# Kernel tuning notes

Hardware: AMD Instinct MI355X
Metric: run time of the kernel (lower is better)

## Reference

```python
import jax, jax.numpy as jnp
import numpy as np
from jax import lax

B, S, C = 64, 256, 12          # sentences, words/sentence, chars/word
Ec, Hc = 50, 64                # char embed / char LSTM hidden (per direction)
Ew = 300                       # word embed dim
Hw = 256 + Hc                  # word LSTM hidden per direction = word_hidden_dim + char_hidden_dim
Din = Ew + 2 * Hc              # word LSTM input dim
NT = 20                        # len(tag_vocab.stoi) - 2
Vw, Vc = 50000, 100


def setup_inputs() -> dict:
    key = jax.random.key(0)
    ks = jax.random.split(key, 32)
    p = lambda i, shape: jax.random.normal(ks[i], shape, jnp.float32) * 0.05
    inp = {
        'batch_sentences': jax.random.randint(ks[0], (B, S), 0, Vw),
        'lengths': jnp.full((B,), S, dtype=jnp.int32),  # sorted (all full) -> packed == time-major
        'char_ids': jax.random.randint(ks[1], (B, S, C), 0, Vc),
        'word_emb': p(2, (Vw, Ew)),
        'char_emb': p(3, (Vc, Ec)),
        'char_h0': p(4, (2, Hc)),  # fixed random init state (init_char_hidden), [fwd/bwd, Hc]
        'char_c0': p(5, (2, Hc)),
        'Wih_cf': p(6, (4 * Hc, Ec)), 'Whh_cf': p(7, (4 * Hc, Hc)), 'bih_cf': p(8, (4 * Hc,)), 'bhh_cf': p(9, (4 * Hc,)),
        'Wih_cb': p(10, (4 * Hc, Ec)), 'Whh_cb': p(11, (4 * Hc, Hc)), 'bih_cb': p(12, (4 * Hc,)), 'bhh_cb': p(13, (4 * Hc,)),
        'Wih_wf': p(14, (4 * Hw, Din)), 'Whh_wf': p(15, (4 * Hw, Hw)), 'bih_wf': p(16, (4 * Hw,)), 'bhh_wf': p(17, (4 * Hw,)),
        'Wih_wb': p(18, (4 * Hw, Din)), 'Whh_wb': p(19, (4 * Hw, Hw)), 'bih_wb': p(20, (4 * Hw,)), 'bhh_wb': p(21, (4 * Hw,)),
        'W_tag': p(22, (NT, 2 * Hw)), 'b_tag': p(23, (NT,)),
    }
    return inp


def _lstm(x, h0, c0, Wih, Whh, bih, bhh):
    """x: [T, N, In] time-major. Returns (all h [T,N,H], final h [N,H]). torch gate order i,f,g,o."""
    pre = jnp.einsum('tni,gi->tng', x, Wih) + bih  # input projection for all steps

    def step(carry, pt):
        h, c = carry
        g = pt + h @ Whh.T + bhh
        i, f, gg, o = jnp.split(g, 4, axis=-1)
        c = jax.nn.sigmoid(f) * c + jax.nn.sigmoid(i) * jnp.tanh(gg)
        h = jax.nn.sigmoid(o) * jnp.tanh(c)
        return (h, c), h

    (hT, _), hs = lax.scan(step, (h0, c0), pre)
    return hs, hT


def reference(batch_sentences, lengths, char_ids, word_emb, char_emb, char_h0, char_c0,
              Wih_cf, Whh_cf, bih_cf, bhh_cf, Wih_cb, Whh_cb, bih_cb, bhh_cb,
              Wih_wf, Whh_wf, bih_wf, bhh_wf, Wih_wb, Whh_wb, bih_wb, bhh_wb,
              W_tag, b_tag):
    N = B * S
    we = word_emb[batch_sentences]                                   # [B,S,Ew]
    ce = char_emb[char_ids].reshape(N, C, Ec).transpose(1, 0, 2)     # [C,N,Ec] all words batched

    bc = lambda v: jnp.broadcast_to(v, (N, Hc))
    _, hTf = _lstm(ce, bc(char_h0[0]), bc(char_c0[0]), Wih_cf, Whh_cf, bih_cf, bhh_cf)
    _, hTb = _lstm(ce[::-1], bc(char_h0[1]), bc(char_c0[1]), Wih_cb, Whh_cb, bih_cb, bhh_cb)
    char_feat = jnp.concatenate([hTf, hTb], -1).reshape(B, S, 2 * Hc)  # hn.view(-1) per word

    x = jnp.concatenate([we, char_feat], -1).transpose(1, 0, 2)      # [S,B,Din] time-major
    z0 = jnp.zeros((B, Hw), x.dtype)
    hsf, _ = _lstm(x, z0, z0, Wih_wf, Whh_wf, bih_wf, bhh_wf)
    hsb, _ = _lstm(x[::-1], z0, z0, Wih_wb, Whh_wb, bih_wb, bhh_wb)
    out = jnp.concatenate([hsf, hsb[::-1]], -1)                      # [S,B,2*Hw]

    # lengths are all == S, so packed data order == time-major flatten
    packed = out.reshape(S * B, 2 * Hw)
    tag_scores = packed @ W_tag.T + b_tag                            # [S*B, NT]
    return tag_scores
```

## Files before the change

kernel.cpp:

```cpp
#include <hip/hip_runtime.h>
#include <stdint.h>

typedef __attribute__((ext_vector_type(8))) short bf16x8;
typedef __attribute__((ext_vector_type(4))) float f32x4;
typedef unsigned short u16;
typedef unsigned int u32;
typedef unsigned long long u64;

#define DEV static __device__ __forceinline__


DEV u16 f2b(float f){ union{float f; u32 u;} v; v.f=f; return (u16)((v.u + 0x7FFFu + ((v.u>>16)&1u))>>16); }
DEV float b2f(u16 b){ union{u32 u; float f;} v; v.u=((u32)b)<<16; return v.f; }
DEV float sigm(float x){ return 1.0f/(1.0f + __expf(-x)); }
DEV float tanhf2(float x){ float a=fabsf(x); float e=__expf(-2.0f*a); float t=(1.0f-e)/(1.0f+e); return x<0.0f? -t : t; }

DEV u32 l2_atomic_add_ret(u32* p, u32 v){
  u32 old;
  asm volatile("global_atomic_add %0, %1, %2, off sc0\n\ts_waitcnt vmcnt(0)"
               : "=v"(old) : "v"(p), "v"(v) : "memory");
  return old;
}
DEV void l2_atomic_add_nr(u32* p, u32 v){
  asm volatile("global_atomic_add %0, %1, off" :: "v"(p), "v"(v) : "memory");
}
DEV void l2_atomic_swap_nr(u32* p, u32 v){
  asm volatile("global_atomic_swap %0, %1, off" :: "v"(p), "v"(v) : "memory");
}

__global__ void k_init(u32* flags){ flags[threadIdx.x] = 0u; }

__global__ __launch_bounds__(256,1) void k_char(
    const int* __restrict__ char_ids, const float* __restrict__ cemb,
    const float* __restrict__ h0g, const float* __restrict__ c0g,
    const float* __restrict__ WihF, const float* __restrict__ WhhF,
    const float* __restrict__ bihF, const float* __restrict__ bhhF,
    const float* __restrict__ WihB, const float* __restrict__ WhhB,
    const float* __restrict__ bihB, const float* __restrict__ bhhB,
    u16* __restrict__ cfF, u16* __restrict__ cfB)
{
  __shared__ __align__(16) u16 Wl[256*128];
  __shared__ __align__(16) u16 Xc[64*128];
  __shared__ __align__(16) u16 Gc[64*256];

  const int dir = blockIdx.x & 1;
  const int n0  = (blockIdx.x >> 1) * 64;
  const int tid = threadIdx.x;
  const int lane = tid & 63, wv = tid >> 6;
  const int l15 = lane & 15, l4 = lane >> 4;

  const float* Wih = dir ? WihB : WihF;
  const float* Whh = dir ? WhhB : WhhF;
  const float* bih = dir ? bihB : bihF;
  const float* bhh = dir ? bhhB : bhhF;
  const float* h0 = h0g + dir*64;
  const float* c0 = c0g + dir*64;

  {
    const int n = tid; const int gt = n & 3, col = n >> 2;
    const int grow = gt*64 + col;
    for (int k = 0; k < 128; ++k){
      float v;
      if (k < 50) v = Wih[grow*50 + k];
      else if (k < 114) v = Whh[grow*64 + (k-50)];
      else if (k == 114) v = bih[grow] + bhh[grow];
      else v = 0.0f;
      Wl[n*128 + (k ^ ((n&7)<<3))] = f2b(v);
    }
  }
  for (int idx = tid; idx < 64*128; idx += 256){
    int w = idx >> 7, k = idx & 127;
    float v = (k==114) ? 1.0f : ((k>=50 && k<114) ? h0[k-50] : 0.0f);
    Xc[w*128 + (k ^ ((w&7)<<3))] = f2b(v);
  }
  const int uw = tid >> 2, ucb = (tid & 3) * 16;
  float cst[16], hreg[16];
  #pragma unroll
  for (int cc = 0; cc < 16; ++cc){ cst[cc] = c0[ucb + cc]; hreg[cc] = 0.0f; }

  for (int t = 0; t < 12; ++t){
    const int cpos = dir ? (11 - t) : t;
    __syncthreads();
    for (int idx = tid; idx < 3200; idx += 256){
      int w = idx / 50, k = idx - w*50;
      int cid = char_ids[(n0 + w)*12 + cpos];
      Xc[w*128 + (k ^ ((w&7)<<3))] = f2b(cemb[cid*50 + k]);
    }
    __syncthreads();
    f32x4 acc[4][4];
    #pragma unroll
    for (int mt=0; mt<4; ++mt)
      #pragma unroll
      for (int nt=0; nt<4; ++nt)
        #pragma unroll
        for (int j=0;j<4;++j) acc[mt][nt][j] = 0.0f;
    #pragma unroll
    for (int kk = 0; kk < 4; ++kk){
      bf16x8 A[4];
      #pragma unroll
      for (int mt=0; mt<4; ++mt){
        int row = mt*16 + l15;
        A[mt] = *(const bf16x8*)&Xc[row*128 + ((kk*32 + 8*l4) ^ ((row&7)<<3))];
      }
      #pragma unroll
      for (int nt=0; nt<4; ++nt){
        int n = wv*64 + nt*16 + l15;
        bf16x8 Bf = *(const bf16x8*)&Wl[n*128 + ((kk*32 + 8*l4) ^ ((n&7)<<3))];
        #pragma unroll
        for (int mt=0; mt<4; ++mt)
          acc[mt][nt] = __builtin_amdgcn_mfma_f32_16x16x32_bf16(A[mt], Bf, acc[mt][nt], 0,0,0);
      }
    }
    #pragma unroll
    for (int mt=0; mt<4; ++mt)
      #pragma unroll
      for (int nt=0; nt<4; ++nt)
        #pragma unroll
        for (int j=0;j<4;++j){
          int m = mt*16 + l4*4 + j;
          int n = wv*64 + nt*16 + l15;
          Gc[m*256 + n] = f2b(acc[mt][nt][j]);
        }
    __syncthreads();
    #pragma unroll
    for (int cc=0; cc<16; ++cc){
      int col = ucb + cc;
      const u16* gp = &Gc[uw*256 + col*4];
      float gi=b2f(gp[0]), gf=b2f(gp[1]), gg=b2f(gp[2]), go=b2f(gp[3]);
      float c2 = sigm(gf)*cst[cc] + sigm(gi)*tanhf2(gg);
      cst[cc]=c2;
      float h = sigm(go)*tanhf2(c2);
      hreg[cc]=h;
      Xc[uw*128 + ((50+col) ^ ((uw&7)<<3))] = f2b(h);
    }
  }
  u16* cf = dir ? cfB : cfF;
  #pragma unroll
  for (int cc=0; cc<16; ++cc) cf[(u64)(n0+uw)*64 + ucb + cc] = f2b(hreg[cc]);
}

__global__ __launch_bounds__(256,1) void k_buildx(
    const int* __restrict__ sents, const float* __restrict__ wemb,
    const u16* __restrict__ cfF, const u16* __restrict__ cfB,
    u16* __restrict__ xg)
{
  const int r = blockIdx.x*4 + (threadIdx.x >> 6);
  const int lane = threadIdx.x & 63;
  const int t = r >> 6, b = r & 63;
  const int sid = sents[b*256 + t];
  const int n = b*256 + t;
  u32* xr = (u32*)(xg + (u64)r*448);
  const float* we = wemb + (u64)sid*300;
  const u16* cf = cfF + (u64)n*64;
  const u16* cb = cfB + (u64)n*64;
  for (int u = lane; u < 224; u += 64){
    int c0 = 2*u, c1 = 2*u + 1;
    u16 lo = (c0 < 300) ? f2b(we[c0]) : (c0 < 364) ? cf[c0-300] : (c0 < 428) ? cb[c0-364] : (c0==428) ? f2b(1.0f) : (u16)0;
    u16 hi = (c1 < 300) ? f2b(we[c1]) : (c1 < 364) ? cf[c1-300] : (c1 < 428) ? cb[c1-364] : (c1==428) ? f2b(1.0f) : (u16)0;
    xr[u] = (u32)lo | ((u32)hi << 16);
  }
}

DEV void stage_x(const u16* __restrict__ src, u16* Xs, int tid)
{
  #pragma unroll
  for (int half=0; half<2; ++half){
    f32x4 r[7];
    #pragma unroll
    for (int p=0;p<7;++p){ int idx=tid+256*(half*7+p); int row=idx/56, e=idx-row*56;
      r[p] = *(const f32x4*)(src + row*448 + e*8); }
    #pragma unroll
    for (int p=0;p<7;++p){ int idx=tid+256*(half*7+p); int row=idx/56, e=idx-row*56;
      *(f32x4*)&Xs[row*456 + e*8] = r[p]; }
  }
}

DEV void wih_mfma(f32x4 (&ACC)[2][4], const u16* Xs, const bf16x8 (&BWih)[2][14],
                  int l15, int l4)
{
  #pragma unroll
  for (int nt=0;nt<2;++nt)
    #pragma unroll
    for (int mt=0;mt<4;++mt)
      #pragma unroll
      for (int j=0;j<4;++j) ACC[nt][mt][j]=0.f;
  #pragma unroll
  for (int kk=0;kk<14;++kk){
    bf16x8 A[4];
    #pragma unroll
    for (int mt=0;mt<4;++mt)
      A[mt] = *(const bf16x8*)&Xs[(mt*16+l15)*456 + kk*32 + 8*l4];
    #pragma unroll
    for (int nt=0;nt<2;++nt)
      #pragma unroll
      for (int mt=0;mt<4;++mt)
        ACC[nt][mt] = __builtin_amdgcn_mfma_f32_16x16x32_bf16(A[mt], BWih[nt][kk], ACC[nt][mt],0,0,0);
  }
}

DEV void fill_bwih(bf16x8 (&BWih)[2][14], const float* Wih, const float* bih,
                   const float* bhh, int wg, int wv, int l15, int l4)
{
  #pragma unroll
  for (int nt=0; nt<2; ++nt){
    const int q = wv*32 + nt*16 + l15;
    const int col = q >> 2, gt = q & 3;
    const int grow = gt*320 + wg*32 + col;
    #pragma unroll
    for (int kk=0; kk<14; ++kk){
      bf16x8 v;
      #pragma unroll
      for (int j=0;j<8;++j){
        int k = kk*32 + 8*l4 + j;
        float f = (k < 428) ? Wih[(u64)grow*428 + k] : ((k==428) ? (bih[grow]+bhh[grow]) : 0.0f);
        v[j] = (short)f2b(f);
      }
      BWih[nt][kk] = v;
    }
  }
}

__global__ __launch_bounds__(256,1) void k_pre(
    const u16* __restrict__ xg,
    const float* __restrict__ WihFg, const float* __restrict__ bihFg, const float* __restrict__ bhhFg,
    const float* __restrict__ WihBg, const float* __restrict__ bihBg, const float* __restrict__ bhhBg,
    float* __restrict__ g0)
{
  __shared__ __align__(16) u16 Xs[64*456];
  const int bid = blockIdx.x;
  const int chunk = bid & 31;
  const int wgdir = bid >> 5;
  const int dir = wgdir / 10, wg = wgdir - dir*10;
  const int tid = threadIdx.x;
  const int lane = tid & 63, wv = tid >> 6;
  const int l15 = lane & 15, l4 = lane >> 4;

  const float* Wih = dir ? WihBg : WihFg;
  const float* bih = dir ? bihBg : bihFg;
  const float* bhh = dir ? bhhBg : bhhFg;

  bf16x8 BWih[2][14];
  fill_bwih(BWih, Wih, bih, bhh, wg, wv, l15, l4);

  f32x4 ACC[2][4];
  for (int tt=0; tt<8; ++tt){
    const int t = chunk*8 + tt;
    stage_x(xg + (u64)t*64*448, Xs, tid);
    __syncthreads();
    wih_mfma(ACC, Xs, BWih, l15, l4);
    float* gb = g0 + ((u64)((dir*256 + t)*10 + wg))*8192 + tid*4;
    #pragma unroll
    for (int nt=0; nt<2; ++nt)
      #pragma unroll
      for (int mt=0; mt<4; ++mt)
        *(f32x4*)(gb + (u64)(nt*4+mt)*1024) = ACC[nt][mt];
    __syncthreads();
  }
}

__global__ __launch_bounds__(256,1) void k_word_fast(
    const float* __restrict__ g0,
    const float* __restrict__ WhhFg, const float* __restrict__ WhhBg,
    u16* __restrict__ h_g, u32* __restrict__ flags, u16* __restrict__ hs)
{
  __shared__ __align__(16) u16 Hs[64*328];
  __shared__ int s_dir, s_wg;

  if (threadIdx.x == 0){
    u32 xcd;
    asm("s_getreg_b32 %0, hwreg(HW_REG_XCC_ID)" : "=s"(xcd));
    xcd &= 7u;
    int dir = -1, wg = 0;
    if (xcd <= 1u){
      u32 slot = atomicAdd(&flags[32 + xcd], 1u);
      if (slot < 10u){ dir = (int)xcd; wg = (int)slot; }
    }
    s_dir = dir; s_wg = wg;
  }
  __syncthreads();
  const int dir = s_dir, wg = s_wg;
  if (dir < 0) return;

  const int tid = threadIdx.x;
  const int lane = tid & 63, wv = tid >> 6;
  const int l15 = lane & 15, l4 = lane >> 4;
  const int qa = l15 & 3, qq = l15 >> 2;

  const float* Whh = dir ? WhhBg : WhhFg;
  u32* ctr = &flags[64 + dir*16];

  bf16x8 BWhh[2][10];
  #pragma unroll
  for (int nt=0; nt<2; ++nt){
    const int q = wv*32 + nt*16 + l15;
    const int col = q >> 2, gt = q & 3;
    const int grow = gt*320 + wg*32 + col;
    #pragma unroll
    for (int kk=0; kk<10; ++kk){
      bf16x8 v;
      #pragma unroll
      for (int j=0;j<8;++j)
        v[j] = (short)f2b(Whh[(u64)grow*320 + kk*32 + 8*l4 + j]);
      BWhh[nt][kk] = v;
    }
  }

  float cst[8];
  #pragma unroll
  for (int p=0;p<8;++p) cst[p]=0.0f;

  f32x4 PF[8];
  {
    const int t0 = dir ? 255 : 0;
    const float* gb = g0 + ((u64)((dir*256 + t0)*10 + wg))*8192 + tid*4;
    #pragma unroll
    for (int j=0;j<8;++j) PF[j] = *(const f32x4*)(gb + (u64)j*1024);
  }

  for (int i=0; i<256; ++i){
    const int t = dir ? 255-i : i;

    f32x4 ACC[2][4];
    #pragma unroll
    for (int nt=0;nt<2;++nt)
      #pragma unroll
      for (int mt=0;mt<4;++mt)
        #pragma unroll
        for (int j=0;j<4;++j) ACC[nt][mt][j]=0.f;

    if (i > 0){
      if (tid == 0){
        const u32 tgt = 10u*(u32)i;
        int guard = 0;
        while (l2_atomic_add_ret(ctr, 0u) < tgt){
          __builtin_amdgcn_s_sleep(1);
          if (++guard > (1<<13)) break;
        }
      }
      __syncthreads();
      asm volatile("buffer_inv" ::: "memory");
      {
        const u16* hb = h_g + (u64)(((i-1)&1)*2 + dir)*64*320;
        #pragma unroll
        for (int p=0; p<10; ++p){
          int idx = tid + 256*p;
          int row = idx / 40, e = idx - row*40;
          f32x4 v = *(const f32x4*)(hb + row*320 + e*8);
          *(f32x4*)&Hs[row*328 + e*8] = v;
        }
      }
      __syncthreads();
      #pragma unroll
      for (int kk=0; kk<10; ++kk){
        bf16x8 A[4];
        #pragma unroll
        for (int mt=0; mt<4; ++mt)
          A[mt] = *(const bf16x8*)&Hs[(mt*16 + l15)*328 + kk*32 + 8*l4];
        #pragma unroll
        for (int nt=0; nt<2; ++nt)
          #pragma unroll
          for (int mt=0; mt<4; ++mt)
            ACC[nt][mt] = __builtin_amdgcn_mfma_f32_16x16x32_bf16(A[mt], BWhh[nt][kk], ACC[nt][mt],0,0,0);
      }
    }

    u64 pk[2][4];
    #pragma unroll
    for (int nt=0; nt<2; ++nt){
      #pragma unroll
      for (int mt=0; mt<4; ++mt){
        f32x4 v = ACC[nt][mt] + PF[nt*4 + mt];
        float t0=__shfl_xor(v[1],1), t1=__shfl_xor(v[0],1), t2=__shfl_xor(v[3],1), t3=__shfl_xor(v[2],1);
        v[0] = (qa&1) ? t0 : v[0];
        v[1] = (qa&1) ? v[1] : t1;
        v[2] = (qa&1) ? t2 : v[2];
        v[3] = (qa&1) ? v[3] : t3;
        float u0=__shfl_xor(v[2],2), u1=__shfl_xor(v[3],2), u2=__shfl_xor(v[0],2), u3=__shfl_xor(v[1],2);
        v[0] = (qa&2) ? u0 : v[0];
        v[1] = (qa&2) ? u1 : v[1];
        v[2] = (qa&2) ? v[2] : u2;
        v[3] = (qa&2) ? v[3] : u3;
        v[0]=b2f(f2b(v[0])); v[1]=b2f(f2b(v[1])); v[2]=b2f(f2b(v[2])); v[3]=b2f(f2b(v[3]));
        const int ci = nt*4 + mt;
        float c2 = sigm(v[1])*cst[ci] + sigm(v[0])*tanhf2(v[2]);
        cst[ci] = c2;
        float h = sigm(v[3])*tanhf2(c2);
        u32 hu = (u32)f2b(h);
        u32 v01 = hu | ((u32)__shfl_xor((int)hu, 4) << 16);
        u32 v23 = (u32)__shfl_xor((int)v01, 8);
        pk[nt][mt] = (u64)v01 | ((u64)v23 << 32);
      }
    }
    {
      u16* hw = h_g + (u64)((i&1)*2 + dir)*64*320;
      if (qq == 0){
        #pragma unroll
        for (int nt=0; nt<2; ++nt)
          #pragma unroll
          for (int mt=0; mt<4; ++mt){
            const int b = mt*16 + l4*4 + qa;
            *(u64*)&hw[b*320 + wg*32 + wv*8 + nt*4] = pk[nt][mt];
          }
      }
    }
    asm volatile("s_waitcnt vmcnt(0)" ::: "memory");
    __syncthreads();
    if (tid == 0) l2_atomic_add_nr(ctr, 1u);
    if (qq == 0){
      #pragma unroll
      for (int nt=0; nt<2; ++nt)
        #pragma unroll
        for (int mt=0; mt<4; ++mt){
          const int b = mt*16 + l4*4 + qa;
          *(u64*)&hs[(u64)(t*64 + b)*640 + dir*320 + wg*32 + wv*8 + nt*4] = pk[nt][mt];
        }
    }
    if (i < 255){
      const int tn = dir ? 254-i : i+1;
      const float* gb = g0 + ((u64)((dir*256 + tn)*10 + wg))*8192 + tid*4;
      #pragma unroll
      for (int j=0;j<8;++j) PF[j] = *(const f32x4*)(gb + (u64)j*1024);
    }
  }
}

DEV void spin_flag(u32* fp, u32 tgt){
  int guard = 0;
  while (l2_atomic_add_ret(fp, 0u) < tgt){
    __builtin_amdgcn_s_sleep(1);
    if (++guard > (1<<13)) break;
  }
}

__global__ __launch_bounds__(256,1) void k_word_slow(
    const u16* __restrict__ xg,
    const float* __restrict__ WihFg, const float* __restrict__ WhhFg,
    const float* __restrict__ bihFg, const float* __restrict__ bhhFg,
    const float* __restrict__ WihBg, const float* __restrict__ WhhBg,
    const float* __restrict__ bihBg, const float* __restrict__ bhhBg,
    u16* __restrict__ h_g, u32* __restrict__ flags, u16* __restrict__ hs)
{
  __shared__ __align__(16) u16 Hs[64*328];
  __shared__ __align__(16) u16 Xs[64*456];
  __shared__ int s_dir, s_wg;

  if (threadIdx.x == 0){
    u32 xcd;
    asm("s_getreg_b32 %0, hwreg(HW_REG_XCC_ID)" : "=s"(xcd));
    xcd &= 7u;
    int dir = -1, wg = 0;
    if (xcd <= 1u){
      u32 slot = atomicAdd(&flags[32 + xcd], 1u);
      if (slot < 10u){ dir = (int)xcd; wg = (int)slot; }
    }
    s_dir = dir; s_wg = wg;
  }
  __syncthreads();
  const int dir = s_dir, wg = s_wg;
  if (dir < 0) return;

  const int tid = threadIdx.x;
  const int lane = tid & 63, wv = tid >> 6;
  const int l15 = lane & 15, l4 = lane >> 4;
  const int qa = l15 & 3, qq = l15 >> 2;

  const float* Wih = dir ? WihBg : WihFg;
  const float* Whh = dir ? WhhBg : WhhFg;
  const float* bih = dir ? bihBg : bihFg;
  const float* bhh = dir ? bhhBg : bhhFg;

  bf16x8 BWih[2][14];
  fill_bwih(BWih, Wih, bih, bhh, wg, wv, l15, l4);
  bf16x8 BWhh[2][10];
  #pragma unroll
  for (int nt=0; nt<2; ++nt){
    const int q = wv*32 + nt*16 + l15;
    const int col = q >> 2, gt = q & 3;
    const int grow = gt*320 + wg*32 + col;
    #pragma unroll
    for (int kk=0; kk<10; ++kk){
      bf16x8 v;
      #pragma unroll
      for (int j=0;j<8;++j)
        v[j] = (short)f2b(Whh[(u64)grow*320 + kk*32 + 8*l4 + j]);
      BWhh[nt][kk] = v;
    }
  }

  float cst[8];
  #pragma unroll
  for (int p=0;p<8;++p) cst[p]=0.0f;

  f32x4 ACC[2][4];
  stage_x(xg + (u64)(dir ? 255 : 0)*64*448, Xs, tid);
  __syncthreads();
  wih_mfma(ACC, Xs, BWih, l15, l4);

  for (int i=0; i<256; ++i){
    const int t = dir ? 255-i : i;
    if (i > 0){
      if (tid < 10) spin_flag(&flags[dir*16 + tid], (u32)i);
      __syncthreads();
      asm volatile("buffer_inv" ::: "memory");
      {
        const u16* hb = h_g + (u64)(((i-1)&1)*2 + dir)*64*320;
        #pragma unroll
        for (int p=0; p<10; ++p){
          int idx = tid + 256*p;
          int row = idx / 40, e = idx - row*40;
          f32x4 v = *(const f32x4*)(hb + row*320 + e*8);
          *(f32x4*)&Hs[row*328 + e*8] = v;
        }
      }
      __syncthreads();
      #pragma unroll
      for (int kk=0; kk<10; ++kk){
        bf16x8 A[4];
        #pragma unroll
        for (int mt=0; mt<4; ++mt)
          A[mt] = *(const bf16x8*)&Hs[(mt*16 + l15)*328 + kk*32 + 8*l4];
        #pragma unroll
        for (int nt=0; nt<2; ++nt)
          #pragma unroll
          for (int mt=0; mt<4; ++mt)
            ACC[nt][mt] = __builtin_amdgcn_mfma_f32_16x16x32_bf16(A[mt], BWhh[nt][kk], ACC[nt][mt],0,0,0);
      }
    }

    u64 pk[2][4];
    #pragma unroll
    for (int nt=0; nt<2; ++nt){
      #pragma unroll
      for (int mt=0; mt<4; ++mt){
        f32x4 v = ACC[nt][mt];
        float t0=__shfl_xor(v[1],1), t1=__shfl_xor(v[0],1), t2=__shfl_xor(v[3],1), t3=__shfl_xor(v[2],1);
        v[0] = (qa&1) ? t0 : v[0];
        v[1] = (qa&1) ? v[1] : t1;
        v[2] = (qa&1) ? t2 : v[2];
        v[3] = (qa&1) ? v[3] : t3;
        float u0=__shfl_xor(v[2],2), u1=__shfl_xor(v[3],2), u2=__shfl_xor(v[0],2), u3=__shfl_xor(v[1],2);
        v[0] = (qa&2) ? u0 : v[0];
        v[1] = (qa&2) ? u1 : v[1];
        v[2] = (qa&2) ? v[2] : u2;
        v[3] = (qa&2) ? v[3] : u3;
        v[0]=b2f(f2b(v[0])); v[1]=b2f(f2b(v[1])); v[2]=b2f(f2b(v[2])); v[3]=b2f(f2b(v[3]));
        const int ci = nt*4 + mt;
        float c2 = sigm(v[1])*cst[ci] + sigm(v[0])*tanhf2(v[2]);
        cst[ci] = c2;
        float h = sigm(v[3])*tanhf2(c2);
        u32 hu = (u32)f2b(h);
        u32 v01 = hu | ((u32)__shfl_xor((int)hu, 4) << 16);
        u32 v23 = (u32)__shfl_xor((int)v01, 8);
        pk[nt][mt] = (u64)v01 | ((u64)v23 << 32);
      }
    }
    {
      u16* hw = h_g + (u64)((i&1)*2 + dir)*64*320;
      if (qq == 0){
        #pragma unroll
        for (int nt=0; nt<2; ++nt)
          #pragma unroll
          for (int mt=0; mt<4; ++mt){
            const int b = mt*16 + l4*4 + qa;
            *(u64*)&hw[b*320 + wg*32 + wv*8 + nt*4] = pk[nt][mt];
          }
      }
    }
    asm volatile("s_waitcnt vmcnt(0)" ::: "memory");
    __syncthreads();
    if (tid == 0) l2_atomic_swap_nr(&flags[dir*16 + wg], (u32)(i+1));
    if (qq == 0){
      #pragma unroll
      for (int nt=0; nt<2; ++nt)
        #pragma unroll
        for (int mt=0; mt<4; ++mt){
          const int b = mt*16 + l4*4 + qa;
          *(u64*)&hs[(u64)(t*64 + b)*640 + dir*320 + wg*32 + wv*8 + nt*4] = pk[nt][mt];
        }
    }
    if (i < 255){
      stage_x(xg + (u64)(dir ? 254-i : i+1)*64*448, Xs, tid);
      __syncthreads();
      wih_mfma(ACC, Xs, BWih, l15, l4);
    }
  }
}

__global__ __launch_bounds__(256,1) void k_tag(
    const u16* __restrict__ hs, const float* __restrict__ Wt,
    const float* __restrict__ bt, float* __restrict__ out)
{
  __shared__ __align__(16) u16 Wl[32*648];
  __shared__ float btl[32];
  const int tid = threadIdx.x;
  const int lane = tid & 63, wv = tid >> 6;
  const int l15 = lane & 15, l4 = lane >> 4;
  const int r0 = blockIdx.x * 64;

  for (int p=0; p<80; ++p){
    int idx = tid + 256*p;
    int nq = idx / 640, k = idx - nq*640;
    Wl[nq*648 + k] = (nq < 20) ? f2b(Wt[(u64)nq*640 + k]) : (u16)0;
  }
  if (tid < 32) btl[tid] = (tid < 20) ? bt[tid] : 0.0f;
  __syncthreads();

  f32x4 acc[2];
  #pragma unroll
  for (int nt=0;nt<2;++nt)
    #pragma unroll
    for (int j=0;j<4;++j) acc[nt][j]=0.0f;

  const int mrow = r0 + wv*16 + l15;
  #pragma unroll
  for (int kk=0; kk<20; ++kk){
    bf16x8 A = *(const bf16x8*)&hs[(u64)mrow*640 + kk*32 + 8*l4];
    #pragma unroll
    for (int nt=0; nt<2; ++nt){
      bf16x8 Bf = *(const bf16x8*)&Wl[(nt*16 + l15)*648 + kk*32 + 8*l4];
      acc[nt] = __builtin_amdgcn_mfma_f32_16x16x32_bf16(A, Bf, acc[nt], 0,0,0);
    }
  }
  #pragma unroll
  for (int nt=0; nt<2; ++nt){
    int nq = nt*16 + l15;
    if (nq < 20){
      #pragma unroll
      for (int j=0;j<4;++j){
        int row = r0 + wv*16 + l4*4 + j;
        out[(u64)row*20 + nq] = acc[nt][j] + btl[nq];
      }
    }
  }
}

extern "C" void kernel_launch(void* const* d_in, const int* in_sizes, int n_in,
                              void* d_out, int out_size, void* d_ws, size_t ws_size,
                              hipStream_t stream)
{
  (void)in_sizes; (void)n_in; (void)out_size;
  const int*   sents   = (const int*)d_in[0];
  const int*   charids = (const int*)d_in[2];
  const float* wemb    = (const float*)d_in[3];
  const float* cemb    = (const float*)d_in[4];
  const float* ch0     = (const float*)d_in[5];
  const float* cc0     = (const float*)d_in[6];
  const float* Wih_cf  = (const float*)d_in[7];
  const float* Whh_cf  = (const float*)d_in[8];
  const float* bih_cf  = (const float*)d_in[9];
  const float* bhh_cf  = (const float*)d_in[10];
  const float* Wih_cb  = (const float*)d_in[11];
  const float* Whh_cb  = (const float*)d_in[12];
  const float* bih_cb  = (const float*)d_in[13];
  const float* bhh_cb  = (const float*)d_in[14];
  const float* Wih_wf  = (const float*)d_in[15];
  const float* Whh_wf  = (const float*)d_in[16];
  const float* bih_wf  = (const float*)d_in[17];
  const float* bhh_wf  = (const float*)d_in[18];
  const float* Wih_wb  = (const float*)d_in[19];
  const float* Whh_wb  = (const float*)d_in[20];
  const float* bih_wb  = (const float*)d_in[21];
  const float* bhh_wb  = (const float*)d_in[22];
  const float* W_tag   = (const float*)d_in[23];
  const float* b_tag   = (const float*)d_in[24];

  char* ws = (char*)d_ws;
  u32* flags = (u32*)(ws);
  u16* h_g   = (u16*)(ws + 1024);
  u16* cf_f  = (u16*)(ws + 164864);
  u16* cf_b  = (u16*)(ws + 2262016);
  u16* x     = (u16*)(ws + 4359168);
  u16* hs    = (u16*)(ws + 19039232);
  float* g0  = (float*)(ws + 40010752);
  const u64 need = 40010752ull + 167772160ull;
  float* outp = (float*)d_out;

  hipLaunchKernelGGL(k_init, dim3(1), dim3(128), 0, stream, flags);
  hipLaunchKernelGGL(k_char, dim3(512), dim3(256), 0, stream,
    charids, cemb, ch0, cc0, Wih_cf, Whh_cf, bih_cf, bhh_cf,
    Wih_cb, Whh_cb, bih_cb, bhh_cb, cf_f, cf_b);
  hipLaunchKernelGGL(k_buildx, dim3(4096), dim3(256), 0, stream, sents, wemb, cf_f, cf_b, x);
  if ((u64)ws_size >= need){
    hipLaunchKernelGGL(k_pre, dim3(640), dim3(256), 0, stream,
      x, Wih_wf, bih_wf, bhh_wf, Wih_wb, bih_wb, bhh_wb, g0);
    hipLaunchKernelGGL(k_word_fast, dim3(256), dim3(256), 0, stream,
      g0, Whh_wf, Whh_wb, h_g, flags, hs);
  } else {
    hipLaunchKernelGGL(k_word_slow, dim3(256), dim3(256), 0, stream,
      x, Wih_wf, Whh_wf, bih_wf, bhh_wf, Wih_wb, Whh_wb, bih_wb, bhh_wb, h_g, flags, hs);
  }
  hipLaunchKernelGGL(k_tag, dim3(256), dim3(256), 0, stream, hs, W_tag, b_tag, outp);
}
```

Baseline: 1.848 ms.

## Replace per-direction step barrier with per-workgroup flags and incremental K-chunk consumption

The word LSTM recurrence now has each workgroup publish its own step flag instead of bumping one shared counter per direction. Consumers start on their own hidden-state slice straight from LDS, then wait per wave on each peer's flag and issue that peer's K-chunk MFMA as soon as it is ready. This is meant to cut the full-group barrier latency and overlap it with partial matmul work. The costs are more flag polling traffic, a shorter spin guard that could silently proceed on stale data, and a larger flag region that shifts the workspace offsets.

```diff
diff --git a/kernel.cpp b/kernel.cpp
--- a/kernel.cpp
+++ b/kernel.cpp
@@ -21,11 +21,20 @@
                : "=v"(old) : "v"(p), "v"(v) : "memory");
   return old;
 }
-DEV void l2_atomic_add_nr(u32* p, u32 v){
-  asm volatile("global_atomic_add %0, %1, off" :: "v"(p), "v"(v) : "memory");
-}
 DEV void l2_atomic_swap_nr(u32* p, u32 v){
   asm volatile("global_atomic_swap %0, %1, off" :: "v"(p), "v"(v) : "memory");
+}
+
+DEV void wave_wait(u32* fp, u32 tgt, int lane){
+  int guard = 0;
+  for (;;){
+    u32 v = 0;
+    if (lane == 0) v = l2_atomic_add_ret(fp, 0u);
+    v = (u32)__shfl((int)v, 0);
+    if (v >= tgt) break;
+    __builtin_amdgcn_s_sleep(1);
+    if (++guard > (1<<10)) break;
+  }
 }
 
 __global__ void k_init(u32* flags){ flags[threadIdx.x] = 0u; }
@@ -287,7 +296,7 @@
   const int qa = l15 & 3, qq = l15 >> 2;
 
   const float* Whh = dir ? WhhBg : WhhFg;
-  u32* ctr = &flags[64 + dir*16];
+  u32* myflag = &flags[256 + (dir*10 + wg)*16];
 
   bf16x8 BWhh[2][10];
   #pragma unroll
@@ -317,52 +326,16 @@
     for (int j=0;j<8;++j) PF[j] = *(const f32x4*)(gb + (u64)j*1024);
   }
 
+  f32x4 ACC[2][4];
+  #pragma unroll
+  for (int nt=0;nt<2;++nt)
+    #pragma unroll
+    for (int mt=0;mt<4;++mt)
+      #pragma unroll
+      for (int j=0;j<4;++j) ACC[nt][mt][j]=0.f;
+
   for (int i=0; i<256; ++i){
     const int t = dir ? 255-i : i;
-
-    f32x4 ACC[2][4];
-    #pragma unroll
-    for (int nt=0;nt<2;++nt)
-      #pragma unroll
-      for (int mt=0;mt<4;++mt)
-        #pragma unroll
-        for (int j=0;j<4;++j) ACC[nt][mt][j]=0.f;
-
-    if (i > 0){
-      if (tid == 0){
-        const u32 tgt = 10u*(u32)i;
-        int guard = 0;
-        while (l2_atomic_add_ret(ctr, 0u) < tgt){
-          __builtin_amdgcn_s_sleep(1);
-          if (++guard > (1<<13)) break;
-        }
-      }
-      __syncthreads();
-      asm volatile("buffer_inv" ::: "memory");
-      {
-        const u16* hb = h_g + (u64)(((i-1)&1)*2 + dir)*64*320;
-        #pragma unroll
-        for (int p=0; p<10; ++p){
-          int idx = tid + 256*p;
-          int row = idx / 40, e = idx - row*40;
-          f32x4 v = *(const f32x4*)(hb + row*320 + e*8);
-          *(f32x4*)&Hs[row*328 + e*8] = v;
-        }
-      }
-      __syncthreads();
-      #pragma unroll
-      for (int kk=0; kk<10; ++kk){
-        bf16x8 A[4];
-        #pragma unroll
-        for (int mt=0; mt<4; ++mt)
-          A[mt] = *(const bf16x8*)&Hs[(mt*16 + l15)*328 + kk*32 + 8*l4];
-        #pragma unroll
-        for (int nt=0; nt<2; ++nt)
-          #pragma unroll
-          for (int mt=0; mt<4; ++mt)
-            ACC[nt][mt] = __builtin_amdgcn_mfma_f32_16x16x32_bf16(A[mt], BWhh[nt][kk], ACC[nt][mt],0,0,0);
-      }
-    }
 
     u64 pk[2][4];
     #pragma unroll
@@ -399,27 +372,57 @@
           #pragma unroll
           for (int mt=0; mt<4; ++mt){
             const int b = mt*16 + l4*4 + qa;
-            *(u64*)&hw[b*320 + wg*32 + wv*8 + nt*4] = pk[nt][mt];
+            const int c = wg*32 + wv*8 + nt*4;
+            *(u64*)&Hs[b*328 + c] = pk[nt][mt];
+            *(u64*)&hw[b*320 + c] = pk[nt][mt];
+            *(u64*)&hs[(u64)(t*64 + b)*640 + dir*320 + c] = pk[nt][mt];
           }
       }
     }
     asm volatile("s_waitcnt vmcnt(0)" ::: "memory");
     __syncthreads();
-    if (tid == 0) l2_atomic_add_nr(ctr, 1u);
-    if (qq == 0){
-      #pragma unroll
-      for (int nt=0; nt<2; ++nt)
-        #pragma unroll
-        for (int mt=0; mt<4; ++mt){
-          const int b = mt*16 + l4*4 + qa;
-          *(u64*)&hs[(u64)(t*64 + b)*640 + dir*320 + wg*32 + wv*8 + nt*4] = pk[nt][mt];
-        }
-    }
+    if (tid == 0) l2_atomic_swap_nr(myflag, (u32)(i+1));
+    asm volatile("buffer_inv" ::: "memory");
+
+    #pragma unroll
+    for (int nt=0;nt<2;++nt)
+      #pragma unroll
+      for (int mt=0;mt<4;++mt)
+        #pragma unroll
+        for (int j=0;j<4;++j) ACC[nt][mt][j]=0.f;
+
     if (i < 255){
-      const int tn = dir ? 254-i : i+1;
-      const float* gb = g0 + ((u64)((dir*256 + tn)*10 + wg))*8192 + tid*4;
-      #pragma unroll
-      for (int j=0;j<8;++j) PF[j] = *(const f32x4*)(gb + (u64)j*1024);
+      {
+        const int tn = dir ? 254-i : i+1;
+        const float* gb = g0 + ((u64)((dir*256 + tn)*10 + wg))*8192 + tid*4;
+        #pragma unroll
+        for (int j=0;j<8;++j) PF[j] = *(const f32x4*)(gb + (u64)j*1024);
+      }
+      {
+        bf16x8 A[4];
+        #pragma unroll
+        for (int mt=0; mt<4; ++mt)
+          A[mt] = *(const bf16x8*)&Hs[(mt*16 + l15)*328 + wg*32 + 8*l4];
+        #pragma unroll
+        for (int nt=0; nt<2; ++nt)
+          #pragma unroll
+          for (int mt=0; mt<4; ++mt)
+            ACC[nt][mt] = __builtin_amdgcn_mfma_f32_16x16x32_bf16(A[mt], BWhh[nt][wg], ACC[nt][mt],0,0,0);
+      }
+      const u16* hb = h_g + (u64)((i&1)*2 + dir)*64*320;
+      for (int d=1; d<10; ++d){
+        int k = wg + d; if (k >= 10) k -= 10;
+        wave_wait(&flags[256 + (dir*10 + k)*16], (u32)(i+1), lane);
+        bf16x8 A[4];
+        #pragma unroll
+        for (int mt=0; mt<4; ++mt)
+          A[mt] = *(const bf16x8*)(hb + (u64)(mt*16 + l15)*320 + k*32 + 8*l4);
+        #pragma unroll
+        for (int nt=0; nt<2; ++nt)
+          #pragma unroll
+          for (int mt=0; mt<4; ++mt)
+            ACC[nt][mt] = __builtin_amdgcn_mfma_f32_16x16x32_bf16(A[mt], BWhh[nt][k], ACC[nt][mt],0,0,0);
+      }
     }
   }
 }
@@ -666,16 +669,16 @@
 
   char* ws = (char*)d_ws;
   u32* flags = (u32*)(ws);
-  u16* h_g   = (u16*)(ws + 1024);
-  u16* cf_f  = (u16*)(ws + 164864);
-  u16* cf_b  = (u16*)(ws + 2262016);
-  u16* x     = (u16*)(ws + 4359168);
-  u16* hs    = (u16*)(ws + 19039232);
-  float* g0  = (float*)(ws + 40010752);
-  const u64 need = 40010752ull + 167772160ull;
+  u16* h_g   = (u16*)(ws + 4096);
+  u16* cf_f  = (u16*)(ws + 167936);
+  u16* cf_b  = (u16*)(ws + 2265088);
+  u16* x     = (u16*)(ws + 4362240);
+  u16* hs    = (u16*)(ws + 19042304);
+  float* g0  = (float*)(ws + 40013824);
+  const u64 need = 40013824ull + 167772160ull;
   float* outp = (float*)d_out;
 
-  hipLaunchKernelGGL(k_init, dim3(1), dim3(128), 0, stream, flags);
+  hipLaunchKernelGGL(k_init, dim3(1), dim3(1024), 0, stream, flags);
   hipLaunchKernelGGL(k_char, dim3(512), dim3(256), 0, stream,
     charids, cemb, ch0, cc0, Wih_cf, Whh_cf, bih_cf, bhh_cf,
     Wih_cb, Whh_cb, bih_cb, bhh_cb, cf_f, cf_b);
```

Result: slower. 3.365 ms (+82.1%).
